# Optimization experiments

Measured on AMD Instinct MI355X. Metric: run time of the kernel, lower is better.

The kernel has to match this reference:

```python
import jax, jax.numpy as jnp
import numpy as np

D_MODEL = 1024
D_K = 64
D_V = 64
H = 16
B = 4
S = 2048
NEG = -1000000000.0


def setup_inputs() -> dict:
    key = jax.random.key(0)
    ks = jax.random.split(key, 6)
    x = jax.random.normal(ks[0], (B, S, D_MODEL), dtype=jnp.float32)
    # mask: 1 = pad, 0 = valid (per module's `mask = 1 - mask` convention)
    mask = jax.random.randint(ks[1], (B, S), 0, 2, dtype=jnp.int32)
    sc = 1.0 / np.sqrt(D_MODEL)
    Wq = jax.random.normal(ks[2], (D_K * H, D_MODEL), dtype=jnp.float32) * sc
    Wk = jax.random.normal(ks[3], (D_K * H, D_MODEL), dtype=jnp.float32) * sc
    Wv = jax.random.normal(ks[4], (D_V * H, D_MODEL), dtype=jnp.float32) * sc
    Wo = jax.random.normal(ks[5], (D_MODEL, D_V * H), dtype=jnp.float32) * (1.0 / np.sqrt(D_V * H))
    return {"x": x, "mask": mask, "Wq": Wq, "Wk": Wk, "Wv": Wv, "Wo": Wo}


def _split_heads(y, h):
    b, s, _ = y.shape
    return y.reshape(b, s, h, -1).transpose(0, 2, 1, 3)  # [B,H,S,d]


def reference(x, mask, Wq, Wk, Wv, Wo):
    # valid = 1 - mask (1 where token is valid); bidirectional pad mask = outer product
    valid = (1 - mask).astype(x.dtype)  # [B,S]
    pair = valid[:, None, :, None] * valid[:, None, None, :]  # [B,1,S,S]
    q = _split_heads(x @ Wq.T, H)  # [B,H,S,dk]
    k = _split_heads(x @ Wk.T, H)
    v = _split_heads(x @ Wv.T, H)
    qk = jnp.einsum("bhqd,bhkd->bhqk", q, k) / jnp.sqrt(jnp.asarray(D_K, x.dtype))
    qk = jnp.where(pair == 0, jnp.asarray(NEG, x.dtype), qk)
    attn = jax.nn.softmax(qk, axis=-1)  # dropout omitted (eval mode)
    heads = jnp.einsum("bhqk,bhkd->bhqd", attn, v)
    concat = heads.transpose(0, 2, 1, 3).reshape(x.shape[0], x.shape[1], -1)
    return concat @ Wo.T
```

## Files before the change

### kernel.cpp

```cpp
#include <hip/hip_runtime.h>
#include <stdint.h>


typedef __bf16 bf16;
typedef __bf16 bf16x8 __attribute__((ext_vector_type(8)));
typedef __bf16 bf16x4 __attribute__((ext_vector_type(4)));
typedef float f32x4 __attribute__((ext_vector_type(4)));
typedef float f32x16 __attribute__((ext_vector_type(16)));

#define DM    1024
#define NH    16
#define SS    2048
#define BB    4
#define NTOK  8192
#define QKVLD 3072
#define LOG2E_DIV8 0.18033688011112042f

__device__ __forceinline__ int swz(int row, int byteoff) {
    return byteoff ^ ((row & 7) << 4);
}
__device__ __forceinline__ float fexp2(float x) {
    float r; asm("v_exp_f32 %0, %1" : "=v"(r) : "v"(x)); return r;
}
__device__ __forceinline__ uint32_t cvtpk(float lo, float hi_) {
    uint32_t r; asm("v_cvt_pk_bf16_f32 %0, %1, %2" : "=v"(r) : "v"(lo), "v"(hi_)); return r;
}
__device__ __forceinline__ void gload_lds16(const void* g, void* l) {
    __builtin_amdgcn_global_load_lds(
        (const __attribute__((address_space(1))) uint32_t*)g,
        (__attribute__((address_space(3))) uint32_t*)l, 16, 0, 0);
}

__global__ void cvt_kernel(const float* __restrict__ in, bf16* __restrict__ out, int n8) {
    int i = blockIdx.x * blockDim.x + threadIdx.x;
    if (i >= n8) return;
    const float4* p = reinterpret_cast<const float4*>(in) + (size_t)i * 2;
    float4 a = p[0], b = p[1];
    bf16x8 o;
    o[0] = (bf16)a.x; o[1] = (bf16)a.y; o[2] = (bf16)a.z; o[3] = (bf16)a.w;
    o[4] = (bf16)b.x; o[5] = (bf16)b.y; o[6] = (bf16)b.z; o[7] = (bf16)b.w;
    reinterpret_cast<bf16x8*>(out)[i] = o;
}

__global__ void wcvt_kernel(const float* __restrict__ wq, const float* __restrict__ wk,
                            const float* __restrict__ wv, const float* __restrict__ wo,
                            bf16* __restrict__ wqkv, bf16* __restrict__ wob) {
    int i = blockIdx.x * blockDim.x + threadIdx.x;
    int seg = i >> 17, off = i & 131071;
    const float* src = (seg == 0) ? wq : (seg == 1) ? wk : (seg == 2) ? wv : wo;
    bf16* dst = (seg < 3) ? (wqkv + (size_t)seg * DM * DM) : wob;
    const float4* p = reinterpret_cast<const float4*>(src) + (size_t)off * 2;
    float4 a = p[0], b = p[1];
    bf16x8 o;
    o[0] = (bf16)a.x; o[1] = (bf16)a.y; o[2] = (bf16)a.z; o[3] = (bf16)a.w;
    o[4] = (bf16)b.x; o[5] = (bf16)b.y; o[6] = (bf16)b.z; o[7] = (bf16)b.w;
    reinterpret_cast<bf16x8*>(dst)[off] = o;
}

__global__ void biasprep_kernel(const int* __restrict__ mask, float* __restrict__ bias) {
    int idx = blockIdx.x * blockDim.x + threadIdx.x;
    if (idx >= 5 * 2048) return;
    int e = idx & 15, hi = (idx >> 4) & 1, hs = (idx >> 5) & 1;
    int kt = (idx >> 6) & 31, b = idx >> 11;
    int key = 32 * hs + 4 * hi + 8 * (e >> 2) + (e & 3);
    float v = 0.f;
    if (b < 4 && mask[b * SS + kt * 64 + key]) v = -__builtin_inff();
    bias[idx] = v;
}

template <typename OT>
__global__ __launch_bounds__(256) void gemm_bt(
    const bf16* __restrict__ A, int lda, const bf16* __restrict__ Bm, OT* __restrict__ C,
    int M, int N, int K)
{
    __shared__ bf16 As[128 * 64];
    __shared__ bf16 Bs[128 * 64];

    const int nwg = gridDim.x * gridDim.y;
    const int wg = blockIdx.y * gridDim.x + blockIdx.x;
    const int nsw = (wg & 7) * (nwg >> 3) + (wg >> 3);
    const int tn = nsw % gridDim.x, tm = nsw / gridDim.x;

    const int tid = threadIdx.x;
    const int lane = tid & 63, wv = tid >> 6;
    const int wr = wv >> 1, wc = wv & 1;
    const int lr = lane & 15, lg = lane >> 4;

    const f32x4 zero = {0.f, 0.f, 0.f, 0.f};
    f32x4 acc[4][4];
#pragma unroll
    for (int mi = 0; mi < 4; ++mi)
#pragma unroll
        for (int ni = 0; ni < 4; ++ni) acc[mi][ni] = zero;

    const char* Abase = (const char*)(A + (size_t)(tm * 128) * lda);
    const char* Bbase = (const char*)(Bm + (size_t)(tn * 128) * K);

    for (int k0 = 0; k0 < K; k0 += 64) {
#pragma unroll
        for (int i = 0; i < 4; ++i) {
            int idx = tid + 256 * i;
            int row = idx >> 3, ch = idx & 7;
            int gcol = (ch * 16) ^ ((row & 7) << 4);
            gload_lds16(Abase + (size_t)row * (lda * 2) + k0 * 2 + gcol, (char*)As + idx * 16);
            gload_lds16(Bbase + (size_t)row * (K * 2) + k0 * 2 + gcol, (char*)Bs + idx * 16);
        }
        __syncthreads();

#pragma unroll
        for (int ks = 0; ks < 2; ++ks) {
            bf16x8 af[4], bfr[4];
#pragma unroll
            for (int mi = 0; mi < 4; ++mi) {
                int row = wr * 64 + mi * 16 + lr;
                af[mi] = *reinterpret_cast<const bf16x8*>(
                    (char*)As + swz(row, row * 128 + ks * 64 + lg * 16));
            }
#pragma unroll
            for (int ni = 0; ni < 4; ++ni) {
                int row = wc * 64 + ni * 16 + lr;
                bfr[ni] = *reinterpret_cast<const bf16x8*>(
                    (char*)Bs + swz(row, row * 128 + ks * 64 + lg * 16));
            }
#pragma unroll
            for (int mi = 0; mi < 4; ++mi)
#pragma unroll
                for (int ni = 0; ni < 4; ++ni)
                    acc[mi][ni] = __builtin_amdgcn_mfma_f32_16x16x32_bf16(
                        af[mi], bfr[ni], acc[mi][ni], 0, 0, 0);
        }
        __syncthreads();
    }

#pragma unroll
    for (int mi = 0; mi < 4; ++mi)
#pragma unroll
        for (int ni = 0; ni < 4; ++ni)
#pragma unroll
            for (int r = 0; r < 4; ++r) {
                int row = tm * 128 + wr * 64 + mi * 16 + lg * 4 + r;
                int col = tn * 128 + wc * 64 + ni * 16 + lr;
                C[(size_t)row * N + col] = (OT)acc[mi][ni][r];
            }
}

__global__ __launch_bounds__(256) void vtrans_kernel(
    const bf16* __restrict__ vb, int ldv, bf16* __restrict__ vT)
{
    const int st = blockIdx.x, bh = blockIdx.y;
    const int b = bh >> 4, h = bh & 15;
    const int tid = threadIdx.x;
    __shared__ bf16 T[64 * 64];
#pragma unroll
    for (int i = 0; i < 2; ++i) {
        int idx = tid + 256 * i;
        int s = idx >> 3, ch = idx & 7;
        bf16x8 v = *reinterpret_cast<const bf16x8*>(
            vb + (size_t)(b * SS + st * 64 + s) * ldv + h * 64 + ch * 8);
        *reinterpret_cast<bf16x8*>((char*)T + swz(s, s * 128 + ch * 16)) = v;
    }
    __syncthreads();
#pragma unroll
    for (int i = 0; i < 2; ++i) {
        int idx = tid + 256 * i;
        int d = idx >> 3, ch = idx & 7;
        bf16x8 o;
#pragma unroll
        for (int j = 0; j < 8; ++j) {
            int s = ch * 8 + j;
            o[j] = *reinterpret_cast<const bf16*>((char*)T + swz(s, s * 128 + d * 2));
        }
        *reinterpret_cast<bf16x8*>(vT + ((size_t)bh * 64 + d) * SS + st * 64 + ch * 8) = o;
    }
}

__global__ __launch_bounds__(256) void attn_kernel(
    const bf16* __restrict__ qkv, const bf16* __restrict__ vT,
    const float* __restrict__ bias, const int* __restrict__ mask,
    bf16* __restrict__ concat)
{
    const int w = blockIdx.x;
    const int nw = (w & 7) * 128 + (w >> 3);
    const int qt = nw & 15, bh = nw >> 4;
    const int b = bh >> 4, h = bh & 15;
    const int tid = threadIdx.x;
    const int lane = tid & 63, wv = tid >> 6;
    const int lq = lane & 31, hi = lane >> 5;

    __shared__ bf16 Ks[2][64 * 64];
    __shared__ bf16 Vs[2][64 * 64];

    const size_t tok0 = (size_t)b * SS;
    const int qrow0 = qt * 128 + wv * 32;

    const int qpad = mask[tok0 + qrow0 + lq];
    bf16x8 qf[4];
    {
        const bf16* qp = qkv + (tok0 + qrow0 + lq) * QKVLD + h * 64 + hi * 8;
#pragma unroll
        for (int ks = 0; ks < 4; ++ks) {
            bf16x8 v = *reinterpret_cast<const bf16x8*>(qp + ks * 16);
#pragma unroll
            for (int j = 0; j < 8; ++j)
                v[j] = qpad ? (bf16)0.f : (bf16)((float)v[j] * LOG2E_DIV8);
            qf[ks] = v;
        }
    }
    const float* bbase = bias + (size_t)(qpad ? 4 : b) * 2048 + hi * 16;

    float mrow = -3e38f, lrow = 0.f;
    f32x16 oA, oB;
#pragma unroll
    for (int e = 0; e < 16; ++e) { oA[e] = 0.f; oB[e] = 0.f; }

    const int srow = tid >> 3, sch = tid & 7;
    const int srow2 = (tid + 256) >> 3;
    const int gc1 = (sch * 16) ^ ((srow & 7) << 4);
    const int gc2 = (sch * 16) ^ ((srow2 & 7) << 4);
    const char* kSrc = (const char*)(qkv + 1024 + h * 64);
    const char* vSrc = (const char*)(vT + (size_t)bh * 64 * SS);
    const size_t kOff1 = (tok0 + srow) * (QKVLD * 2) + gc1;
    const size_t kOff2 = (tok0 + srow2) * (QKVLD * 2) + gc2;
    const size_t vOff1 = (size_t)srow * (SS * 2) + gc1;
    const size_t vOff2 = (size_t)srow2 * (SS * 2) + gc2;
    const int ldsOff1 = tid * 16, ldsOff2 = (tid + 256) * 16;
    const int cx = (hi * 16) ^ ((lq & 7) << 4);

    gload_lds16(kSrc + kOff1, (char*)Ks[0] + ldsOff1);
    gload_lds16(kSrc + kOff2, (char*)Ks[0] + ldsOff2);
    gload_lds16(vSrc + vOff1, (char*)Vs[0] + ldsOff1);
    gload_lds16(vSrc + vOff2, (char*)Vs[0] + ldsOff2);
    __syncthreads();

    for (int kt = 0; kt < 32; ++kt) {
        const int cur = kt & 1;

        f32x16 s0 = *reinterpret_cast<const f32x16*>(bbase + kt * 64);
        f32x16 s1 = *reinterpret_cast<const f32x16*>(bbase + kt * 64 + 32);

        if (kt < 31) {
            const size_t kAdv = (size_t)(kt + 1) * 64 * (QKVLD * 2);
            const size_t vAdv = (size_t)(kt + 1) * 128;
            gload_lds16(kSrc + kOff1 + kAdv, (char*)Ks[cur ^ 1] + ldsOff1);
            gload_lds16(kSrc + kOff2 + kAdv, (char*)Ks[cur ^ 1] + ldsOff2);
            gload_lds16(vSrc + vOff1 + vAdv, (char*)Vs[cur ^ 1] + ldsOff1);
            gload_lds16(vSrc + vOff2 + vAdv, (char*)Vs[cur ^ 1] + ldsOff2);
        }

        const char* kB = (const char*)Ks[cur];
        const char* vB = (const char*)Vs[cur];
        const int off0 = lq * 128 + cx, off1 = (32 + lq) * 128 + cx;

        __builtin_amdgcn_s_setprio(1);
#pragma unroll
        for (int ks = 0; ks < 4; ++ks) {
            bf16x8 k0 = *reinterpret_cast<const bf16x8*>(kB + (off0 ^ (ks * 32)));
            bf16x8 k1 = *reinterpret_cast<const bf16x8*>(kB + (off1 ^ (ks * 32)));
            s0 = __builtin_amdgcn_mfma_f32_32x32x16_bf16(k0, qf[ks], s0, 0, 0, 0);
            s1 = __builtin_amdgcn_mfma_f32_32x32x16_bf16(k1, qf[ks], s1, 0, 0, 0);
        }
        __builtin_amdgcn_s_setprio(0);

        float pm = fmaxf(s0[0], s0[1]);
#pragma unroll
        for (int e = 2; e < 16; e += 2) pm = fmaxf(pm, fmaxf(s0[e], s0[e + 1]));
#pragma unroll
        for (int e = 0; e < 16; e += 2) pm = fmaxf(pm, fmaxf(s1[e], s1[e + 1]));
        pm = fmaxf(pm, __shfl_xor(pm, 32));

        if (!__all(pm <= mrow + 11.0f)) {
            float mnew = fmaxf(mrow, pm);
            float scf = fexp2(mrow - mnew);
            mrow = mnew;
            lrow *= scf;
#pragma unroll
            for (int e = 0; e < 16; ++e) { oA[e] *= scf; oB[e] *= scf; }
        }

        float p0[16], p1[16];
        float ps0 = 0.f, ps1 = 0.f, ps2 = 0.f, ps3 = 0.f;
#pragma unroll
        for (int e = 0; e < 16; e += 2) {
            p0[e] = fexp2(s0[e] - mrow);     ps0 += p0[e];
            p0[e + 1] = fexp2(s0[e + 1] - mrow); ps1 += p0[e + 1];
            p1[e] = fexp2(s1[e] - mrow);     ps2 += p1[e];
            p1[e + 1] = fexp2(s1[e + 1] - mrow); ps3 += p1[e + 1];
        }
        float psum = (ps0 + ps1) + (ps2 + ps3);
        psum += __shfl_xor(psum, 32);
        lrow += psum;

        __builtin_amdgcn_s_setprio(1);
#pragma unroll
        for (int kk = 0; kk < 4; ++kk) {
            const float* pp = (kk < 2) ? p0 : p1;
            const int ks2 = kk & 1;
            uint32_t c0 = cvtpk(pp[8 * ks2 + 0], pp[8 * ks2 + 1]);
            uint32_t c1 = cvtpk(pp[8 * ks2 + 2], pp[8 * ks2 + 3]);
            uint32_t c2 = cvtpk(pp[8 * ks2 + 4], pp[8 * ks2 + 5]);
            uint32_t c3 = cvtpk(pp[8 * ks2 + 6], pp[8 * ks2 + 7]);
            asm("v_permlane32_swap_b32 %0, %1" : "+v"(c0), "+v"(c2));
            asm("v_permlane32_swap_b32 %0, %1" : "+v"(c1), "+v"(c3));
            union { uint32_t u[4]; bf16x8 v; } pu;
            pu.u[0] = c0; pu.u[1] = c1; pu.u[2] = c2; pu.u[3] = c3;
            bf16x8 vf0 = *reinterpret_cast<const bf16x8*>(vB + (off0 ^ (kk * 32)));
            bf16x8 vf1 = *reinterpret_cast<const bf16x8*>(vB + (off1 ^ (kk * 32)));
            oA = __builtin_amdgcn_mfma_f32_32x32x16_bf16(vf0, pu.v, oA, 0, 0, 0);
            oB = __builtin_amdgcn_mfma_f32_32x32x16_bf16(vf1, pu.v, oB, 0, 0, 0);
        }
        __builtin_amdgcn_s_setprio(0);

        if (kt < 31) __syncthreads();
    }

    float inv = 1.0f / lrow;
#pragma unroll
    for (int g = 0; g < 4; ++g) {
        bf16x4 w0, w1;
#pragma unroll
        for (int r = 0; r < 4; ++r) {
            w0[r] = (bf16)(oA[g * 4 + r] * inv);
            w1[r] = (bf16)(oB[g * 4 + r] * inv);
        }
        int d0 = 4 * hi + 8 * g;
        bf16* cp = concat + (tok0 + qrow0 + lq) * QKVLD + h * 64 + d0;
        *reinterpret_cast<bf16x4*>(cp) = w0;
        *reinterpret_cast<bf16x4*>(cp + 32) = w1;
    }
}

extern "C" void kernel_launch(void* const* d_in, const int* in_sizes, int n_in,
                              void* d_out, int out_size, void* d_ws, size_t ws_size,
                              hipStream_t stream)
{
    const float* x  = (const float*)d_in[0];
    const int* mask = (const int*)d_in[1];
    const float* Wq = (const float*)d_in[2];
    const float* Wk = (const float*)d_in[3];
    const float* Wv = (const float*)d_in[4];
    const float* Wo = (const float*)d_in[5];
    float* out = (float*)d_out;

    char* ws = (char*)d_ws;
    bf16* xb    = (bf16*)(ws);
    bf16* wqkv  = (bf16*)(ws + (16ull << 20));
    bf16* wob   = (bf16*)(ws + (22ull << 20));
    bf16* qkv   = (bf16*)(ws + (24ull << 20));
    bf16* vT    = xb;
    float* bias = (float*)wqkv;
    bf16* concat = qkv + 2048;

    cvt_kernel<<<dim3((NTOK * DM / 8) / 256), 256, 0, stream>>>(x, xb, NTOK * DM / 8);
    wcvt_kernel<<<dim3(2048), 256, 0, stream>>>(Wq, Wk, Wv, Wo, wqkv, wob);

    gemm_bt<bf16><<<dim3(QKVLD / 128, NTOK / 128), 256, 0, stream>>>(
        xb, DM, wqkv, qkv, NTOK, QKVLD, DM);

    vtrans_kernel<<<dim3(SS / 64, BB * NH), 256, 0, stream>>>(qkv + 2048, QKVLD, vT);
    biasprep_kernel<<<dim3(40), 256, 0, stream>>>(mask, bias);

    attn_kernel<<<dim3((SS / 128) * (BB * NH)), 256, 0, stream>>>(
        qkv, vT, bias, mask, concat);

    gemm_bt<float><<<dim3(DM / 128, NTOK / 128), 256, 0, stream>>>(
        concat, QKVLD, wob, out, NTOK, DM, DM);
}
```

Before: 226.6 us.

## Enlarge attention tiles to 256 queries and 128 keys, stage mask bias in LDS

The attention kernel now runs 512-thread blocks covering 256 query rows, and each iteration processes 128-key K/V tiles, so the loop runs 16 times instead of 32. Each loaded K/V tile is shared by twice as many waves, and there are half as many barriers and loop overheads. The per-batch mask bias is copied once into LDS, with a zero slot for padded query rows, instead of being read from global memory every iteration. In exchange, LDS use and register pressure per block rise, and there are half as many blocks (512), which may lower occupancy.

New measurement: 206.0 us. 9.1% less time.

```diff
diff --git a/kernel.cpp b/kernel.cpp
--- a/kernel.cpp
+++ b/kernel.cpp
@@ -59,13 +59,11 @@
 
 __global__ void biasprep_kernel(const int* __restrict__ mask, float* __restrict__ bias) {
     int idx = blockIdx.x * blockDim.x + threadIdx.x;
-    if (idx >= 5 * 2048) return;
-    int e = idx & 15, hi = (idx >> 4) & 1, hs = (idx >> 5) & 1;
-    int kt = (idx >> 6) & 31, b = idx >> 11;
-    int key = 32 * hs + 4 * hi + 8 * (e >> 2) + (e & 3);
-    float v = 0.f;
-    if (b < 4 && mask[b * SS + kt * 64 + key]) v = -__builtin_inff();
-    bias[idx] = v;
+    if (idx >= 4 * 2048) return;
+    int e = idx & 15, hi = (idx >> 4) & 1, kg = (idx >> 5) & 3;
+    int kt = (idx >> 7) & 15, b = idx >> 11;
+    int key = kt * 128 + kg * 32 + 4 * hi + 8 * (e >> 2) + (e & 3);
+    bias[idx] = mask[b * SS + key] ? -__builtin_inff() : 0.f;
 }
 
 template <typename OT>
@@ -174,24 +172,25 @@
     }
 }
 
-__global__ __launch_bounds__(256) void attn_kernel(
+__global__ __launch_bounds__(512) void attn_kernel(
     const bf16* __restrict__ qkv, const bf16* __restrict__ vT,
     const float* __restrict__ bias, const int* __restrict__ mask,
     bf16* __restrict__ concat)
 {
     const int w = blockIdx.x;
-    const int nw = (w & 7) * 128 + (w >> 3);
-    const int qt = nw & 15, bh = nw >> 4;
+    const int nw = (w & 7) * 64 + (w >> 3);
+    const int qt = nw & 7, bh = nw >> 3;
     const int b = bh >> 4, h = bh & 15;
     const int tid = threadIdx.x;
     const int lane = tid & 63, wv = tid >> 6;
     const int lq = lane & 31, hi = lane >> 5;
 
-    __shared__ bf16 Ks[2][64 * 64];
-    __shared__ bf16 Vs[2][64 * 64];
+    __shared__ bf16 Ks[2][128 * 64];
+    __shared__ bf16 Vs[2][64 * 128];
+    __shared__ float Bl[2048 + 16];
 
     const size_t tok0 = (size_t)b * SS;
-    const int qrow0 = qt * 128 + wv * 32;
+    const int qrow0 = qt * 256 + wv * 32;
 
     const int qpad = mask[tok0 + qrow0 + lq];
     bf16x8 qf[4];
@@ -206,66 +205,76 @@
             qf[ks] = v;
         }
     }
-    const float* bbase = bias + (size_t)(qpad ? 4 : b) * 2048 + hi * 16;
 
     float mrow = -3e38f, lrow = 0.f;
     f32x16 oA, oB;
 #pragma unroll
     for (int e = 0; e < 16; ++e) { oA[e] = 0.f; oB[e] = 0.f; }
 
-    const int srow = tid >> 3, sch = tid & 7;
-    const int srow2 = (tid + 256) >> 3;
-    const int gc1 = (sch * 16) ^ ((srow & 7) << 4);
-    const int gc2 = (sch * 16) ^ ((srow2 & 7) << 4);
+    const int c0 = tid, c1 = tid + 512;
+    const int kr0 = c0 >> 3, kc0 = c0 & 7, kr1 = c1 >> 3, kc1 = c1 & 7;
+    const int vr0 = c0 >> 4, vc0 = c0 & 15, vr1 = c1 >> 4, vc1 = c1 & 15;
     const char* kSrc = (const char*)(qkv + 1024 + h * 64);
     const char* vSrc = (const char*)(vT + (size_t)bh * 64 * SS);
-    const size_t kOff1 = (tok0 + srow) * (QKVLD * 2) + gc1;
-    const size_t kOff2 = (tok0 + srow2) * (QKVLD * 2) + gc2;
-    const size_t vOff1 = (size_t)srow * (SS * 2) + gc1;
-    const size_t vOff2 = (size_t)srow2 * (SS * 2) + gc2;
-    const int ldsOff1 = tid * 16, ldsOff2 = (tid + 256) * 16;
-    const int cx = (hi * 16) ^ ((lq & 7) << 4);
-
-    gload_lds16(kSrc + kOff1, (char*)Ks[0] + ldsOff1);
-    gload_lds16(kSrc + kOff2, (char*)Ks[0] + ldsOff2);
-    gload_lds16(vSrc + vOff1, (char*)Vs[0] + ldsOff1);
-    gload_lds16(vSrc + vOff2, (char*)Vs[0] + ldsOff2);
+    const size_t kOff0 = (tok0 + kr0) * (QKVLD * 2) + ((kc0 * 16) ^ ((kr0 & 7) << 4));
+    const size_t kOff1 = (tok0 + kr1) * (QKVLD * 2) + ((kc1 * 16) ^ ((kr1 & 7) << 4));
+    const size_t vOff0 = (size_t)vr0 * (SS * 2) + ((vc0 * 16) ^ ((vr0 & 15) << 4));
+    const size_t vOff1 = (size_t)vr1 * (SS * 2) + ((vc1 * 16) ^ ((vr1 & 15) << 4));
+
+    const int kxor = (hi * 16) ^ ((lq & 7) << 4);
+    const int vxor = (hi * 16) ^ ((lq & 15) << 4);
+    const int bmask = qpad ? 0 : -1;
+    const char* bbase = (const char*)Bl + (qpad ? 8192 : hi * 64);
+
+    gload_lds16(kSrc + kOff0, (char*)Ks[0] + c0 * 16);
+    gload_lds16(kSrc + kOff1, (char*)Ks[0] + c1 * 16);
+    gload_lds16(vSrc + vOff0, (char*)Vs[0] + c0 * 16);
+    gload_lds16(vSrc + vOff1, (char*)Vs[0] + c1 * 16);
+    gload_lds16((const char*)(bias + (size_t)b * 2048) + tid * 16, (char*)Bl + tid * 16);
+    if (tid < 4) {
+        f32x4 z = {0.f, 0.f, 0.f, 0.f};
+        *reinterpret_cast<f32x4*>((char*)Bl + 8192 + tid * 16) = z;
+    }
     __syncthreads();
 
-    for (int kt = 0; kt < 32; ++kt) {
+    for (int kt = 0; kt < 16; ++kt) {
         const int cur = kt & 1;
 
-        f32x16 s0 = *reinterpret_cast<const f32x16*>(bbase + kt * 64);
-        f32x16 s1 = *reinterpret_cast<const f32x16*>(bbase + kt * 64 + 32);
-
-        if (kt < 31) {
-            const size_t kAdv = (size_t)(kt + 1) * 64 * (QKVLD * 2);
-            const size_t vAdv = (size_t)(kt + 1) * 128;
-            gload_lds16(kSrc + kOff1 + kAdv, (char*)Ks[cur ^ 1] + ldsOff1);
-            gload_lds16(kSrc + kOff2 + kAdv, (char*)Ks[cur ^ 1] + ldsOff2);
-            gload_lds16(vSrc + vOff1 + vAdv, (char*)Vs[cur ^ 1] + ldsOff1);
-            gload_lds16(vSrc + vOff2 + vAdv, (char*)Vs[cur ^ 1] + ldsOff2);
+        if (kt < 15) {
+            const size_t kAdv = (size_t)(kt + 1) * 128 * (QKVLD * 2);
+            const size_t vAdv = (size_t)(kt + 1) * 256;
+            gload_lds16(kSrc + kOff0 + kAdv, (char*)Ks[cur ^ 1] + c0 * 16);
+            gload_lds16(kSrc + kOff1 + kAdv, (char*)Ks[cur ^ 1] + c1 * 16);
+            gload_lds16(vSrc + vOff0 + vAdv, (char*)Vs[cur ^ 1] + c0 * 16);
+            gload_lds16(vSrc + vOff1 + vAdv, (char*)Vs[cur ^ 1] + c1 * 16);
         }
 
         const char* kB = (const char*)Ks[cur];
         const char* vB = (const char*)Vs[cur];
-        const int off0 = lq * 128 + cx, off1 = (32 + lq) * 128 + cx;
-
+        const int bo = (kt * 512) & bmask;
+
+        f32x16 s[4];
+#pragma unroll
+        for (int kg = 0; kg < 4; ++kg)
+            s[kg] = *reinterpret_cast<const f32x16*>(bbase + bo + ((kg * 128) & bmask));
         __builtin_amdgcn_s_setprio(1);
 #pragma unroll
-        for (int ks = 0; ks < 4; ++ks) {
-            bf16x8 k0 = *reinterpret_cast<const bf16x8*>(kB + (off0 ^ (ks * 32)));
-            bf16x8 k1 = *reinterpret_cast<const bf16x8*>(kB + (off1 ^ (ks * 32)));
-            s0 = __builtin_amdgcn_mfma_f32_32x32x16_bf16(k0, qf[ks], s0, 0, 0, 0);
-            s1 = __builtin_amdgcn_mfma_f32_32x32x16_bf16(k1, qf[ks], s1, 0, 0, 0);
+        for (int kg = 0; kg < 4; ++kg) {
+            const char* kR = kB + (kg * 32 + lq) * 128;
+#pragma unroll
+            for (int ks = 0; ks < 4; ++ks) {
+                bf16x8 kf = *reinterpret_cast<const bf16x8*>(kR + (kxor ^ (ks * 32)));
+                s[kg] = __builtin_amdgcn_mfma_f32_32x32x16_bf16(kf, qf[ks], s[kg], 0, 0, 0);
+            }
         }
         __builtin_amdgcn_s_setprio(0);
 
-        float pm = fmaxf(s0[0], s0[1]);
-#pragma unroll
-        for (int e = 2; e < 16; e += 2) pm = fmaxf(pm, fmaxf(s0[e], s0[e + 1]));
-#pragma unroll
-        for (int e = 0; e < 16; e += 2) pm = fmaxf(pm, fmaxf(s1[e], s1[e + 1]));
+        float pm = fmaxf(s[0][0], s[0][1]);
+#pragma unroll
+        for (int kg = 0; kg < 4; ++kg)
+#pragma unroll
+            for (int e = (kg == 0 ? 2 : 0); e < 16; e += 2)
+                pm = fmaxf(pm, fmaxf(s[kg][e], s[kg][e + 1]));
         pm = fmaxf(pm, __shfl_xor(pm, 32));
 
         if (!__all(pm <= mrow + 11.0f)) {
@@ -277,40 +286,44 @@
             for (int e = 0; e < 16; ++e) { oA[e] *= scf; oB[e] *= scf; }
         }
 
-        float p0[16], p1[16];
+        float p[4][16];
         float ps0 = 0.f, ps1 = 0.f, ps2 = 0.f, ps3 = 0.f;
 #pragma unroll
-        for (int e = 0; e < 16; e += 2) {
-            p0[e] = fexp2(s0[e] - mrow);     ps0 += p0[e];
-            p0[e + 1] = fexp2(s0[e + 1] - mrow); ps1 += p0[e + 1];
-            p1[e] = fexp2(s1[e] - mrow);     ps2 += p1[e];
-            p1[e + 1] = fexp2(s1[e + 1] - mrow); ps3 += p1[e + 1];
-        }
+        for (int kg = 0; kg < 4; ++kg)
+#pragma unroll
+            for (int e = 0; e < 16; e += 4) {
+                p[kg][e]     = fexp2(s[kg][e] - mrow);     ps0 += p[kg][e];
+                p[kg][e + 1] = fexp2(s[kg][e + 1] - mrow); ps1 += p[kg][e + 1];
+                p[kg][e + 2] = fexp2(s[kg][e + 2] - mrow); ps2 += p[kg][e + 2];
+                p[kg][e + 3] = fexp2(s[kg][e + 3] - mrow); ps3 += p[kg][e + 3];
+            }
         float psum = (ps0 + ps1) + (ps2 + ps3);
         psum += __shfl_xor(psum, 32);
         lrow += psum;
 
         __builtin_amdgcn_s_setprio(1);
 #pragma unroll
-        for (int kk = 0; kk < 4; ++kk) {
-            const float* pp = (kk < 2) ? p0 : p1;
+        for (int kk = 0; kk < 8; ++kk) {
+            const float* pp = p[kk >> 1];
             const int ks2 = kk & 1;
-            uint32_t c0 = cvtpk(pp[8 * ks2 + 0], pp[8 * ks2 + 1]);
-            uint32_t c1 = cvtpk(pp[8 * ks2 + 2], pp[8 * ks2 + 3]);
-            uint32_t c2 = cvtpk(pp[8 * ks2 + 4], pp[8 * ks2 + 5]);
-            uint32_t c3 = cvtpk(pp[8 * ks2 + 6], pp[8 * ks2 + 7]);
-            asm("v_permlane32_swap_b32 %0, %1" : "+v"(c0), "+v"(c2));
-            asm("v_permlane32_swap_b32 %0, %1" : "+v"(c1), "+v"(c3));
+            uint32_t c0p = cvtpk(pp[8 * ks2 + 0], pp[8 * ks2 + 1]);
+            uint32_t c1p = cvtpk(pp[8 * ks2 + 2], pp[8 * ks2 + 3]);
+            uint32_t c2p = cvtpk(pp[8 * ks2 + 4], pp[8 * ks2 + 5]);
+            uint32_t c3p = cvtpk(pp[8 * ks2 + 6], pp[8 * ks2 + 7]);
+            asm("v_permlane32_swap_b32 %0, %1" : "+v"(c0p), "+v"(c2p));
+            asm("v_permlane32_swap_b32 %0, %1" : "+v"(c1p), "+v"(c3p));
             union { uint32_t u[4]; bf16x8 v; } pu;
-            pu.u[0] = c0; pu.u[1] = c1; pu.u[2] = c2; pu.u[3] = c3;
-            bf16x8 vf0 = *reinterpret_cast<const bf16x8*>(vB + (off0 ^ (kk * 32)));
-            bf16x8 vf1 = *reinterpret_cast<const bf16x8*>(vB + (off1 ^ (kk * 32)));
+            pu.u[0] = c0p; pu.u[1] = c1p; pu.u[2] = c2p; pu.u[3] = c3p;
+            bf16x8 vf0 = *reinterpret_cast<const bf16x8*>(
+                vB + (lq)*256 + (vxor ^ (kk * 32)));
+            bf16x8 vf1 = *reinterpret_cast<const bf16x8*>(
+                vB + (32 + lq) * 256 + (vxor ^ (kk * 32)));
             oA = __builtin_amdgcn_mfma_f32_32x32x16_bf16(vf0, pu.v, oA, 0, 0, 0);
             oB = __builtin_amdgcn_mfma_f32_32x32x16_bf16(vf1, pu.v, oB, 0, 0, 0);
         }
         __builtin_amdgcn_s_setprio(0);
 
-        if (kt < 31) __syncthreads();
+        if (kt < 15) __syncthreads();
     }
 
     float inv = 1.0f / lrow;
@@ -357,9 +370,9 @@
         xb, DM, wqkv, qkv, NTOK, QKVLD, DM);
 
     vtrans_kernel<<<dim3(SS / 64, BB * NH), 256, 0, stream>>>(qkv + 2048, QKVLD, vT);
-    biasprep_kernel<<<dim3(40), 256, 0, stream>>>(mask, bias);
-
-    attn_kernel<<<dim3((SS / 128) * (BB * NH)), 256, 0, stream>>>(
+    biasprep_kernel<<<dim3(32), 256, 0, stream>>>(mask, bias);
+
+    attn_kernel<<<dim3((SS / 256) * (BB * NH)), 512, 0, stream>>>(
         qkv, vT, bias, mask, concat);
 
     gemm_bt<float><<<dim3(DM / 128, NTOK / 128), 256, 0, stream>>>(
```
